# Performance work log

Measured on AMD Instinct MI355X. Metric: run time of the kernel, lower is better.

Reference implementation:

```python
import jax, jax.numpy as jnp
import numpy as np

B, C, H, W = 4, 256, 48, 48
NUM_HEADS = 8
INTER = C // 2          # squeeze_ratio = 2
HEAD_DIM = INTER // NUM_HEADS


def setup_inputs() -> dict:
    key = jax.random.key(0)
    ks = jax.random.split(key, 11)
    s_in = 1.0 / np.sqrt(C)      # torch Conv2d default init scale (uniform bound)
    s_mid = 1.0 / np.sqrt(INTER)
    return {
        "rgb":   jax.random.normal(ks[0], (B, C, H, W), jnp.float32),
        "depth": jax.random.normal(ks[1], (B, C, H, W), jnp.float32),
        "rgbd":  jax.random.normal(ks[2], (B, C, H, W), jnp.float32),
        # 1x1 convs == channel matmuls; store as [out, in] plus bias
        "Wq": jax.random.uniform(ks[3], (INTER, C), jnp.float32, -s_in, s_in),
        "bq": jax.random.uniform(ks[4], (INTER,), jnp.float32, -s_in, s_in),
        "Wk": jax.random.uniform(ks[5], (INTER, C), jnp.float32, -s_in, s_in),
        "bk": jax.random.uniform(ks[6], (INTER,), jnp.float32, -s_in, s_in),
        "Wv": jax.random.uniform(ks[7], (INTER, C), jnp.float32, -s_in, s_in),
        "bv": jax.random.uniform(ks[8], (INTER,), jnp.float32, -s_in, s_in),
        "Wo": jax.random.uniform(ks[9], (C, INTER), jnp.float32, -s_mid, s_mid),
        "bo": jax.random.uniform(ks[10], (C,), jnp.float32, -s_mid, s_mid),
    }


def _proj(x, Wm, bm):
    # 1x1 conv: [B,Cin,H,W] -> [B,Cout,H,W]
    return jnp.einsum('oc,bchw->bohw', Wm, x) + bm[None, :, None, None]


def reference(rgb, depth, rgbd, Wq, bq, Wk, bk, Wv, bv, Wo, bo):
    P = H * W
    # project and split heads: [B, heads, head_dim, P]
    Q = _proj(rgb, Wq, bq).reshape(B, NUM_HEADS, HEAD_DIM, P)
    K = _proj(depth, Wk, bk).reshape(B, NUM_HEADS, HEAD_DIM, P)
    V = _proj(rgbd, Wv, bv).reshape(B, NUM_HEADS, HEAD_DIM, P)
    scale = 1.0 / np.sqrt(HEAD_DIM)
    # scores [B, heads, P(q), P(k)]
    scores = jnp.einsum('bhdq,bhdk->bhqk', Q, K) * scale
    attn = jax.nn.softmax(scores, axis=-1)
    # output [B, heads, head_dim, P(q)] -> [B, INTER, H, W]
    out = jnp.einsum('bhqk,bhdk->bhdq', attn, V).reshape(B, INTER, H, W)
    refined = _proj(out, Wo, bo)
    return (rgb + refined, depth + refined, rgbd + refined)
```

## Files before the change

kernel.cpp:

```cpp
#include <hip/hip_runtime.h>
#include <stdint.h>

#define P_TOT 2304
#define C_IN  256
#define INTER 128
#define NH    8
#define HD    16
#define QSCALE 0.36067376022224087f

typedef short sh4 __attribute__((ext_vector_type(4)));
typedef short sh8 __attribute__((ext_vector_type(8)));
typedef float fl4 __attribute__((ext_vector_type(4)));

static __device__ __forceinline__ unsigned short f2bf(float f) {
    union { float f; unsigned u; } v; v.f = f;
    return (unsigned short)((v.u + 0x7fffu + ((v.u >> 16) & 1u)) >> 16);
}
static __device__ __forceinline__ unsigned pack_bf2(float a, float b) {
    union { float f; unsigned u; } x, y; x.f = a; y.f = b;
    return __builtin_amdgcn_perm(y.u + 0x8000u, x.u + 0x8000u, 0x07060302u);
}
static __device__ __forceinline__ unsigned pack_bf2_trunc(float a, float b) {
    union { float f; unsigned u; } x, y; x.f = a; y.f = b;
    return __builtin_amdgcn_perm(y.u, x.u, 0x07060302u);
}

__global__ __launch_bounds__(256) void k_prep(
    const float* __restrict__ Wq, const float* __restrict__ Wk,
    const float* __restrict__ Wv, const float* __restrict__ Wo,
    unsigned short* __restrict__ Wb) {
    int i = blockIdx.x * 256 + threadIdx.x;
    int seg = i >> 15, off = i & 32767;
    const float* s = (seg == 0 ? Wq : (seg == 1 ? Wk : (seg == 2 ? Wv : Wo)));
    Wb[i] = f2bf(s[off]);
}

__global__ __launch_bounds__(128) void k_qkv(
    const float* __restrict__ rgb, const float* __restrict__ depth,
    const float* __restrict__ rgbd, const unsigned short* __restrict__ Wb,
    const float* __restrict__ bq, const float* __restrict__ bk,
    const float* __restrict__ bv,
    unsigned short* __restrict__ Qt, unsigned short* __restrict__ Kt,
    unsigned short* __restrict__ Vn) {
    int nt = blockIdx.x, pb = blockIdx.y;
    int pr = pb >> 2, b = pb & 3;
    const unsigned short* W = Wb + pr * (INTER * C_IN);
    const float* bias = (pr == 0 ? bq : (pr == 1 ? bk : bv));
    const float* X = (pr == 0 ? rgb : (pr == 1 ? depth : rgbd)) + (size_t)b * C_IN * P_TOT;
    int tid = threadIdx.x, w = tid >> 6, lane = tid & 63;
    int l15 = lane & 15, quad = lane >> 4;
    int p = nt * 32 + w * 16 + l15;
    fl4 zero = {0.f, 0.f, 0.f, 0.f};
    fl4 acc[8];
#pragma unroll
    for (int i = 0; i < 8; ++i) acc[i] = zero;
    const float* xcol = X + p;
    if (pr < 2) {
#pragma unroll
        for (int k0 = 0; k0 < C_IN; k0 += 32) {
            int cb = k0 + quad * 8;
            unsigned u[8];
#pragma unroll
            for (int j = 0; j < 8; ++j) {
                union { float f; unsigned uu; } t;
                t.f = xcol[(size_t)(cb + j) * P_TOT];
                u[j] = t.uu;
            }
            sh8 bfr;
            unsigned* bu = (unsigned*)&bfr;
            bu[0] = __builtin_amdgcn_perm(u[1] + 0x8000u, u[0] + 0x8000u, 0x07060302u);
            bu[1] = __builtin_amdgcn_perm(u[3] + 0x8000u, u[2] + 0x8000u, 0x07060302u);
            bu[2] = __builtin_amdgcn_perm(u[5] + 0x8000u, u[4] + 0x8000u, 0x07060302u);
            bu[3] = __builtin_amdgcn_perm(u[7] + 0x8000u, u[6] + 0x8000u, 0x07060302u);
#pragma unroll
            for (int mf = 0; mf < 8; ++mf) {
                sh8 af = *(const sh8*)(W + (size_t)(mf * 16 + l15) * C_IN + k0 + quad * 8);
                acc[mf] = __builtin_amdgcn_mfma_f32_16x16x32_bf16(af, bfr, acc[mf], 0, 0, 0);
            }
        }
        unsigned short* dst0 = (pr == 0 ? Qt : Kt);
        float sc = (pr == 0 ? QSCALE : 1.0f);
#pragma unroll
        for (int mf = 0; mf < 8; ++mf) {
            float4 bb = *(const float4*)(bias + mf * 16 + quad * 4);
            uint2 v;
            v.x = pack_bf2((acc[mf][0] + bb.x) * sc, (acc[mf][1] + bb.y) * sc);
            v.y = pack_bf2((acc[mf][2] + bb.z) * sc, (acc[mf][3] + bb.w) * sc);
            *(uint2*)(dst0 + ((size_t)(b * NH + mf) * P_TOT + p) * HD + quad * 4) = v;
        }
    } else {
#pragma unroll
        for (int k0 = 0; k0 < C_IN; k0 += 32) {
            int cb = k0 + quad * 8;
            unsigned u[8];
#pragma unroll
            for (int j = 0; j < 8; ++j) {
                union { float f; unsigned uu; } t;
                t.f = xcol[(size_t)(cb + j) * P_TOT];
                u[j] = t.uu;
            }
            sh8 bfr;
            unsigned* bu = (unsigned*)&bfr;
            bu[0] = __builtin_amdgcn_perm(u[1] + 0x8000u, u[0] + 0x8000u, 0x07060302u);
            bu[1] = __builtin_amdgcn_perm(u[3] + 0x8000u, u[2] + 0x8000u, 0x07060302u);
            bu[2] = __builtin_amdgcn_perm(u[5] + 0x8000u, u[4] + 0x8000u, 0x07060302u);
            bu[3] = __builtin_amdgcn_perm(u[7] + 0x8000u, u[6] + 0x8000u, 0x07060302u);
#pragma unroll
            for (int mf = 0; mf < 8; ++mf) {
                sh8 af = *(const sh8*)(W + (size_t)(mf * 16 + l15) * C_IN + k0 + quad * 8);
                acc[mf] = __builtin_amdgcn_mfma_f32_16x16x32_bf16(bfr, af, acc[mf], 0, 0, 0);
            }
        }
        int pv = nt * 32 + w * 16 + quad * 4;
#pragma unroll
        for (int mf = 0; mf < 8; ++mf) {
            float bb = bias[mf * 16 + l15];
            uint2 v;
            v.x = pack_bf2(acc[mf][0] + bb, acc[mf][1] + bb);
            v.y = pack_bf2(acc[mf][2] + bb, acc[mf][3] + bb);
            *(uint2*)(Vn + ((size_t)(b * NH + mf) * HD + l15) * P_TOT + pv) = v;
        }
    }
}

__global__ __launch_bounds__(256) void k_attn(
    const unsigned short* __restrict__ Qt, const unsigned short* __restrict__ Kt,
    const unsigned short* __restrict__ Vn, unsigned short* __restrict__ Ot) {
    __shared__ fl4 ldsO[4][3][64];
    __shared__ fl4 ldsL[3][64];
    int qt = blockIdx.x, h = blockIdx.y, b = blockIdx.z;
    int tid = threadIdx.x, w = tid >> 6, lane = tid & 63;
    int l15 = lane & 15, quad = lane >> 4;
    int bh = b * NH + h;
    int q0 = qt * 64 + l15;
    const unsigned short* qb = Qt + (size_t)bh * P_TOT * HD + quad * 4;
    sh4 qf0 = *(const sh4*)(qb + (size_t)q0 * HD);
    sh4 qf1 = *(const sh4*)(qb + (size_t)(q0 + 16) * HD);
    sh4 qf2 = *(const sh4*)(qb + (size_t)(q0 + 32) * HD);
    sh4 qf3 = *(const sh4*)(qb + (size_t)(q0 + 48) * HD);
    int ko = w * (P_TOT / 4);
    const unsigned short* kb = Kt + (size_t)bh * P_TOT * HD + quad * 4;
    const unsigned short* vb = Vn + ((size_t)bh * HD + l15) * P_TOT + quad * 4;
    fl4 zero = {0.f, 0.f, 0.f, 0.f};
    fl4 o0 = zero, o1 = zero, o2 = zero, o3 = zero;
    fl4 ls = zero;
    for (int kp = ko; kp < ko + P_TOT / 4; kp += 16) {
        sh4 kf = *(const sh4*)(kb + (size_t)(kp + l15) * HD);
        sh4 vf = *(const sh4*)(vb + kp);
        fl4 s0 = __builtin_amdgcn_mfma_f32_16x16x16bf16_1k(kf, qf0, zero, 0, 0, 0);
        fl4 s1 = __builtin_amdgcn_mfma_f32_16x16x16bf16_1k(kf, qf1, zero, 0, 0, 0);
        fl4 s2 = __builtin_amdgcn_mfma_f32_16x16x16bf16_1k(kf, qf2, zero, 0, 0, 0);
        fl4 s3 = __builtin_amdgcn_mfma_f32_16x16x16bf16_1k(kf, qf3, zero, 0, 0, 0);
        float e00 = __builtin_amdgcn_exp2f(s0[0]), e01 = __builtin_amdgcn_exp2f(s0[1]);
        float e02 = __builtin_amdgcn_exp2f(s0[2]), e03 = __builtin_amdgcn_exp2f(s0[3]);
        float e10 = __builtin_amdgcn_exp2f(s1[0]), e11 = __builtin_amdgcn_exp2f(s1[1]);
        float e12 = __builtin_amdgcn_exp2f(s1[2]), e13 = __builtin_amdgcn_exp2f(s1[3]);
        float e20 = __builtin_amdgcn_exp2f(s2[0]), e21 = __builtin_amdgcn_exp2f(s2[1]);
        float e22 = __builtin_amdgcn_exp2f(s2[2]), e23 = __builtin_amdgcn_exp2f(s2[3]);
        float e30 = __builtin_amdgcn_exp2f(s3[0]), e31 = __builtin_amdgcn_exp2f(s3[1]);
        float e32 = __builtin_amdgcn_exp2f(s3[2]), e33 = __builtin_amdgcn_exp2f(s3[3]);
        ls[0] += (e00 + e01) + (e02 + e03);
        ls[1] += (e10 + e11) + (e12 + e13);
        ls[2] += (e20 + e21) + (e22 + e23);
        ls[3] += (e30 + e31) + (e32 + e33);
        sh4 pf0, pf1, pf2, pf3;
        ((unsigned*)&pf0)[0] = pack_bf2_trunc(e00, e01);
        ((unsigned*)&pf0)[1] = pack_bf2_trunc(e02, e03);
        ((unsigned*)&pf1)[0] = pack_bf2_trunc(e10, e11);
        ((unsigned*)&pf1)[1] = pack_bf2_trunc(e12, e13);
        ((unsigned*)&pf2)[0] = pack_bf2_trunc(e20, e21);
        ((unsigned*)&pf2)[1] = pack_bf2_trunc(e22, e23);
        ((unsigned*)&pf3)[0] = pack_bf2_trunc(e30, e31);
        ((unsigned*)&pf3)[1] = pack_bf2_trunc(e32, e33);
        o0 = __builtin_amdgcn_mfma_f32_16x16x16bf16_1k(vf, pf0, o0, 0, 0, 0);
        o1 = __builtin_amdgcn_mfma_f32_16x16x16bf16_1k(vf, pf1, o1, 0, 0, 0);
        o2 = __builtin_amdgcn_mfma_f32_16x16x16bf16_1k(vf, pf2, o2, 0, 0, 0);
        o3 = __builtin_amdgcn_mfma_f32_16x16x16bf16_1k(vf, pf3, o3, 0, 0, 0);
    }
    if (w > 0) {
        ldsO[0][w - 1][lane] = o0;
        ldsO[1][w - 1][lane] = o1;
        ldsO[2][w - 1][lane] = o2;
        ldsO[3][w - 1][lane] = o3;
        ldsL[w - 1][lane] = ls;
    }
    __syncthreads();
    if (w > 0) return;
#pragma unroll
    for (int s = 0; s < 3; ++s) {
        o0 += ldsO[0][s][lane];
        o1 += ldsO[1][s][lane];
        o2 += ldsO[2][s][lane];
        o3 += ldsO[3][s][lane];
        ls += ldsL[s][lane];
    }
#pragma unroll
    for (int i = 0; i < 4; ++i) {
        ls[i] += __shfl_xor(ls[i], 16);
        ls[i] += __shfl_xor(ls[i], 32);
    }
    float i0 = 1.f / ls[0], i1 = 1.f / ls[1], i2 = 1.f / ls[2], i3 = 1.f / ls[3];
    unsigned short* ob = Ot + (size_t)bh * P_TOT * HD + quad * 4;
    uint2 v;
    v.x = pack_bf2(o0[0] * i0, o0[1] * i0); v.y = pack_bf2(o0[2] * i0, o0[3] * i0);
    *(uint2*)(ob + (size_t)q0 * HD) = v;
    v.x = pack_bf2(o1[0] * i1, o1[1] * i1); v.y = pack_bf2(o1[2] * i1, o1[3] * i1);
    *(uint2*)(ob + (size_t)(q0 + 16) * HD) = v;
    v.x = pack_bf2(o2[0] * i2, o2[1] * i2); v.y = pack_bf2(o2[2] * i2, o2[3] * i2);
    *(uint2*)(ob + (size_t)(q0 + 32) * HD) = v;
    v.x = pack_bf2(o3[0] * i3, o3[1] * i3); v.y = pack_bf2(o3[2] * i3, o3[3] * i3);
    *(uint2*)(ob + (size_t)(q0 + 48) * HD) = v;
}

__global__ __launch_bounds__(128) void k_out(
    const unsigned short* __restrict__ Ot, const unsigned short* __restrict__ Wob,
    const float* __restrict__ bo, const float* __restrict__ rgb,
    const float* __restrict__ depth, const float* __restrict__ rgbd,
    float* __restrict__ out) {
    int nt = blockIdx.x, by = blockIdx.y;
    int cz = by >> 2, b = by & 3;
    int tid = threadIdx.x, w = tid >> 6, lane = tid & 63;
    int l15 = lane & 15, quad = lane >> 4;
    int p0 = nt * 16;
    fl4 zero = {0.f, 0.f, 0.f, 0.f};
    fl4 acc[4];
#pragma unroll
    for (int i = 0; i < 4; ++i) acc[i] = zero;
#pragma unroll
    for (int k0 = 0; k0 < INTER; k0 += 32) {
        int h = (k0 >> 4) + (quad >> 1);
        int doff = 8 * (quad & 1);
        sh8 bfr = *(const sh8*)(Ot + ((size_t)(b * NH + h) * P_TOT + p0 + l15) * HD + doff);
#pragma unroll
        for (int mf2 = 0; mf2 < 4; ++mf2) {
            int mf = (cz * 2 + w) * 4 + mf2;
            sh8 af = *(const sh8*)(Wob + (size_t)(mf * 16 + l15) * INTER + k0 + quad * 8);
            acc[mf2] = __builtin_amdgcn_mfma_f32_16x16x32_bf16(bfr, af, acc[mf2], 0, 0, 0);
        }
    }
    const size_t outsz = (size_t)4 * C_IN * P_TOT;
#pragma unroll
    for (int mf2 = 0; mf2 < 4; ++mf2) {
        int ch = ((cz * 2 + w) * 4 + mf2) * 16 + l15;
        float bb = bo[ch];
        size_t idx = ((size_t)b * C_IN + ch) * P_TOT + p0 + quad * 4;
        float r0 = acc[mf2][0] + bb, r1 = acc[mf2][1] + bb;
        float r2 = acc[mf2][2] + bb, r3 = acc[mf2][3] + bb;
        float4 a = *(const float4*)(rgb + idx);
        float4 d = *(const float4*)(depth + idx);
        float4 g = *(const float4*)(rgbd + idx);
        float4 o;
        o.x = a.x + r0; o.y = a.y + r1; o.z = a.z + r2; o.w = a.w + r3;
        *(float4*)(out + idx) = o;
        o.x = d.x + r0; o.y = d.y + r1; o.z = d.z + r2; o.w = d.w + r3;
        *(float4*)(out + outsz + idx) = o;
        o.x = g.x + r0; o.y = g.y + r1; o.z = g.z + r2; o.w = g.w + r3;
        *(float4*)(out + 2 * outsz + idx) = o;
    }
}

extern "C" void kernel_launch(void* const* d_in, const int* in_sizes, int n_in,
                              void* d_out, int out_size, void* d_ws, size_t ws_size,
                              hipStream_t stream) {
    (void)in_sizes; (void)n_in; (void)out_size; (void)ws_size;
    const float* rgb   = (const float*)d_in[0];
    const float* depth = (const float*)d_in[1];
    const float* rgbd  = (const float*)d_in[2];
    const float* Wq = (const float*)d_in[3];
    const float* bq = (const float*)d_in[4];
    const float* Wk = (const float*)d_in[5];
    const float* bk = (const float*)d_in[6];
    const float* Wv = (const float*)d_in[7];
    const float* bv = (const float*)d_in[8];
    const float* Wo = (const float*)d_in[9];
    const float* bo = (const float*)d_in[10];

    float* outp = (float*)d_out;
    unsigned short* Qt = (unsigned short*)d_out;
    unsigned short* Kt = Qt + (size_t)4 * P_TOT * INTER;
    unsigned short* Vn = Kt + (size_t)4 * P_TOT * INTER;
    unsigned short* Ot = (unsigned short*)d_ws;
    unsigned short* Wb = Ot + (size_t)4 * P_TOT * INTER;

    k_prep<<<512, 256, 0, stream>>>(Wq, Wk, Wv, Wo, Wb);
    k_qkv<<<dim3(72, 12), 128, 0, stream>>>(rgb, depth, rgbd, Wb, bq, bk, bv, Qt, Kt, Vn);
    k_attn<<<dim3(36, NH, 4), 256, 0, stream>>>(Qt, Kt, Vn, Ot);
    k_out<<<dim3(144, 8), 128, 0, stream>>>(Ot, Wb + 3 * 32768, bo, rgb, depth, rgbd, outp);
}
```

Baseline: 173.5 us.

## Split QKV reduction across waves, prefetch K/V in attention, widen out-proj parallelism

```diff
diff --git a/kernel.cpp b/kernel.cpp
--- a/kernel.cpp
+++ b/kernel.cpp
@@ -35,49 +35,69 @@
     Wb[i] = f2bf(s[off]);
 }
 
-__global__ __launch_bounds__(128) void k_qkv(
+__global__ __launch_bounds__(256) void k_qkv(
     const float* __restrict__ rgb, const float* __restrict__ depth,
     const float* __restrict__ rgbd, const unsigned short* __restrict__ Wb,
     const float* __restrict__ bq, const float* __restrict__ bk,
     const float* __restrict__ bv,
     unsigned short* __restrict__ Qt, unsigned short* __restrict__ Kt,
     unsigned short* __restrict__ Vn) {
+    __shared__ fl4 ldsA[2][8][64];
     int nt = blockIdx.x, pb = blockIdx.y;
     int pr = pb >> 2, b = pb & 3;
     const unsigned short* W = Wb + pr * (INTER * C_IN);
     const float* bias = (pr == 0 ? bq : (pr == 1 ? bk : bv));
     const float* X = (pr == 0 ? rgb : (pr == 1 ? depth : rgbd)) + (size_t)b * C_IN * P_TOT;
     int tid = threadIdx.x, w = tid >> 6, lane = tid & 63;
+    int wp = w & 1, chalf = w >> 1;
     int l15 = lane & 15, quad = lane >> 4;
-    int p = nt * 32 + w * 16 + l15;
+    int p = nt * 32 + wp * 16 + l15;
     fl4 zero = {0.f, 0.f, 0.f, 0.f};
     fl4 acc[8];
 #pragma unroll
     for (int i = 0; i < 8; ++i) acc[i] = zero;
     const float* xcol = X + p;
-    if (pr < 2) {
-#pragma unroll
-        for (int k0 = 0; k0 < C_IN; k0 += 32) {
-            int cb = k0 + quad * 8;
-            unsigned u[8];
-#pragma unroll
-            for (int j = 0; j < 8; ++j) {
-                union { float f; unsigned uu; } t;
-                t.f = xcol[(size_t)(cb + j) * P_TOT];
-                u[j] = t.uu;
-            }
-            sh8 bfr;
-            unsigned* bu = (unsigned*)&bfr;
-            bu[0] = __builtin_amdgcn_perm(u[1] + 0x8000u, u[0] + 0x8000u, 0x07060302u);
-            bu[1] = __builtin_amdgcn_perm(u[3] + 0x8000u, u[2] + 0x8000u, 0x07060302u);
-            bu[2] = __builtin_amdgcn_perm(u[5] + 0x8000u, u[4] + 0x8000u, 0x07060302u);
-            bu[3] = __builtin_amdgcn_perm(u[7] + 0x8000u, u[6] + 0x8000u, 0x07060302u);
+    int kbeg = chalf * 128;
+#pragma unroll
+    for (int kk = 0; kk < 128; kk += 32) {
+        int k0 = kbeg + kk;
+        int cb = k0 + quad * 8;
+        unsigned u[8];
+#pragma unroll
+        for (int j = 0; j < 8; ++j) {
+            union { float f; unsigned uu; } t;
+            t.f = xcol[(size_t)(cb + j) * P_TOT];
+            u[j] = t.uu;
+        }
+        sh8 bfr;
+        unsigned* bu = (unsigned*)&bfr;
+        bu[0] = __builtin_amdgcn_perm(u[1] + 0x8000u, u[0] + 0x8000u, 0x07060302u);
+        bu[1] = __builtin_amdgcn_perm(u[3] + 0x8000u, u[2] + 0x8000u, 0x07060302u);
+        bu[2] = __builtin_amdgcn_perm(u[5] + 0x8000u, u[4] + 0x8000u, 0x07060302u);
+        bu[3] = __builtin_amdgcn_perm(u[7] + 0x8000u, u[6] + 0x8000u, 0x07060302u);
+        if (pr < 2) {
 #pragma unroll
             for (int mf = 0; mf < 8; ++mf) {
                 sh8 af = *(const sh8*)(W + (size_t)(mf * 16 + l15) * C_IN + k0 + quad * 8);
                 acc[mf] = __builtin_amdgcn_mfma_f32_16x16x32_bf16(af, bfr, acc[mf], 0, 0, 0);
             }
-        }
+        } else {
+#pragma unroll
+            for (int mf = 0; mf < 8; ++mf) {
+                sh8 af = *(const sh8*)(W + (size_t)(mf * 16 + l15) * C_IN + k0 + quad * 8);
+                acc[mf] = __builtin_amdgcn_mfma_f32_16x16x32_bf16(bfr, af, acc[mf], 0, 0, 0);
+            }
+        }
+    }
+    if (chalf == 1) {
+#pragma unroll
+        for (int mf = 0; mf < 8; ++mf) ldsA[wp][mf][lane] = acc[mf];
+    }
+    __syncthreads();
+    if (chalf == 1) return;
+#pragma unroll
+    for (int mf = 0; mf < 8; ++mf) acc[mf] += ldsA[wp][mf][lane];
+    if (pr < 2) {
         unsigned short* dst0 = (pr == 0 ? Qt : Kt);
         float sc = (pr == 0 ? QSCALE : 1.0f);
 #pragma unroll
@@ -89,29 +109,7 @@
             *(uint2*)(dst0 + ((size_t)(b * NH + mf) * P_TOT + p) * HD + quad * 4) = v;
         }
     } else {
-#pragma unroll
-        for (int k0 = 0; k0 < C_IN; k0 += 32) {
-            int cb = k0 + quad * 8;
-            unsigned u[8];
-#pragma unroll
-            for (int j = 0; j < 8; ++j) {
-                union { float f; unsigned uu; } t;
-                t.f = xcol[(size_t)(cb + j) * P_TOT];
-                u[j] = t.uu;
-            }
-            sh8 bfr;
-            unsigned* bu = (unsigned*)&bfr;
-            bu[0] = __builtin_amdgcn_perm(u[1] + 0x8000u, u[0] + 0x8000u, 0x07060302u);
-            bu[1] = __builtin_amdgcn_perm(u[3] + 0x8000u, u[2] + 0x8000u, 0x07060302u);
-            bu[2] = __builtin_amdgcn_perm(u[5] + 0x8000u, u[4] + 0x8000u, 0x07060302u);
-            bu[3] = __builtin_amdgcn_perm(u[7] + 0x8000u, u[6] + 0x8000u, 0x07060302u);
-#pragma unroll
-            for (int mf = 0; mf < 8; ++mf) {
-                sh8 af = *(const sh8*)(W + (size_t)(mf * 16 + l15) * C_IN + k0 + quad * 8);
-                acc[mf] = __builtin_amdgcn_mfma_f32_16x16x32_bf16(bfr, af, acc[mf], 0, 0, 0);
-            }
-        }
-        int pv = nt * 32 + w * 16 + quad * 4;
+        int pv = nt * 32 + wp * 16 + quad * 4;
 #pragma unroll
         for (int mf = 0; mf < 8; ++mf) {
             float bb = bias[mf * 16 + l15];
@@ -139,14 +137,18 @@
     sh4 qf2 = *(const sh4*)(qb + (size_t)(q0 + 32) * HD);
     sh4 qf3 = *(const sh4*)(qb + (size_t)(q0 + 48) * HD);
     int ko = w * (P_TOT / 4);
-    const unsigned short* kb = Kt + (size_t)bh * P_TOT * HD + quad * 4;
-    const unsigned short* vb = Vn + ((size_t)bh * HD + l15) * P_TOT + quad * 4;
+    const unsigned short* kb = Kt + (size_t)bh * P_TOT * HD + (size_t)(ko + l15) * HD + quad * 4;
+    const unsigned short* vb = Vn + ((size_t)bh * HD + l15) * P_TOT + quad * 4 + ko;
     fl4 zero = {0.f, 0.f, 0.f, 0.f};
     fl4 o0 = zero, o1 = zero, o2 = zero, o3 = zero;
     fl4 ls = zero;
-    for (int kp = ko; kp < ko + P_TOT / 4; kp += 16) {
-        sh4 kf = *(const sh4*)(kb + (size_t)(kp + l15) * HD);
-        sh4 vf = *(const sh4*)(vb + kp);
+    const int NIT = P_TOT / 4 / 16;
+    sh4 kf = *(const sh4*)kb;
+    sh4 vf = *(const sh4*)vb;
+    for (int it = 0; it < NIT; ++it) {
+        int nx = (it + 1 < NIT) ? it + 1 : it;
+        sh4 kf_n = *(const sh4*)(kb + (size_t)nx * 16 * HD);
+        sh4 vf_n = *(const sh4*)(vb + nx * 16);
         fl4 s0 = __builtin_amdgcn_mfma_f32_16x16x16bf16_1k(kf, qf0, zero, 0, 0, 0);
         fl4 s1 = __builtin_amdgcn_mfma_f32_16x16x16bf16_1k(kf, qf1, zero, 0, 0, 0);
         fl4 s2 = __builtin_amdgcn_mfma_f32_16x16x16bf16_1k(kf, qf2, zero, 0, 0, 0);
@@ -176,6 +178,8 @@
         o1 = __builtin_amdgcn_mfma_f32_16x16x16bf16_1k(vf, pf1, o1, 0, 0, 0);
         o2 = __builtin_amdgcn_mfma_f32_16x16x16bf16_1k(vf, pf2, o2, 0, 0, 0);
         o3 = __builtin_amdgcn_mfma_f32_16x16x16bf16_1k(vf, pf3, o3, 0, 0, 0);
+        kf = kf_n;
+        vf = vf_n;
     }
     if (w > 0) {
         ldsO[0][w - 1][lane] = o0;
@@ -212,51 +216,41 @@
     *(uint2*)(ob + (size_t)(q0 + 48) * HD) = v;
 }
 
-__global__ __launch_bounds__(128) void k_out(
+__global__ __launch_bounds__(256) void k_out(
     const unsigned short* __restrict__ Ot, const unsigned short* __restrict__ Wob,
     const float* __restrict__ bo, const float* __restrict__ rgb,
     const float* __restrict__ depth, const float* __restrict__ rgbd,
     float* __restrict__ out) {
-    int nt = blockIdx.x, by = blockIdx.y;
-    int cz = by >> 2, b = by & 3;
+    int nt = blockIdx.x, mg = blockIdx.y, b = blockIdx.z;
     int tid = threadIdx.x, w = tid >> 6, lane = tid & 63;
     int l15 = lane & 15, quad = lane >> 4;
+    int mf = mg * 4 + w;
     int p0 = nt * 16;
     fl4 zero = {0.f, 0.f, 0.f, 0.f};
-    fl4 acc[4];
-#pragma unroll
-    for (int i = 0; i < 4; ++i) acc[i] = zero;
+    fl4 acc = zero;
 #pragma unroll
     for (int k0 = 0; k0 < INTER; k0 += 32) {
         int h = (k0 >> 4) + (quad >> 1);
         int doff = 8 * (quad & 1);
         sh8 bfr = *(const sh8*)(Ot + ((size_t)(b * NH + h) * P_TOT + p0 + l15) * HD + doff);
-#pragma unroll
-        for (int mf2 = 0; mf2 < 4; ++mf2) {
-            int mf = (cz * 2 + w) * 4 + mf2;
-            sh8 af = *(const sh8*)(Wob + (size_t)(mf * 16 + l15) * INTER + k0 + quad * 8);
-            acc[mf2] = __builtin_amdgcn_mfma_f32_16x16x32_bf16(bfr, af, acc[mf2], 0, 0, 0);
-        }
+        sh8 af = *(const sh8*)(Wob + (size_t)(mf * 16 + l15) * INTER + k0 + quad * 8);
+        acc = __builtin_amdgcn_mfma_f32_16x16x32_bf16(bfr, af, acc, 0, 0, 0);
     }
     const size_t outsz = (size_t)4 * C_IN * P_TOT;
-#pragma unroll
-    for (int mf2 = 0; mf2 < 4; ++mf2) {
-        int ch = ((cz * 2 + w) * 4 + mf2) * 16 + l15;
-        float bb = bo[ch];
-        size_t idx = ((size_t)b * C_IN + ch) * P_TOT + p0 + quad * 4;
-        float r0 = acc[mf2][0] + bb, r1 = acc[mf2][1] + bb;
-        float r2 = acc[mf2][2] + bb, r3 = acc[mf2][3] + bb;
-        float4 a = *(const float4*)(rgb + idx);
-        float4 d = *(const float4*)(depth + idx);
-        float4 g = *(const float4*)(rgbd + idx);
-        float4 o;
-        o.x = a.x + r0; o.y = a.y + r1; o.z = a.z + r2; o.w = a.w + r3;
-        *(float4*)(out + idx) = o;
-        o.x = d.x + r0; o.y = d.y + r1; o.z = d.z + r2; o.w = d.w + r3;
-        *(float4*)(out + outsz + idx) = o;
-        o.x = g.x + r0; o.y = g.y + r1; o.z = g.z + r2; o.w = g.w + r3;
-        *(float4*)(out + 2 * outsz + idx) = o;
-    }
+    int ch = mf * 16 + l15;
+    float bb = bo[ch];
+    size_t idx = ((size_t)b * C_IN + ch) * P_TOT + p0 + quad * 4;
+    float r0 = acc[0] + bb, r1 = acc[1] + bb, r2 = acc[2] + bb, r3 = acc[3] + bb;
+    float4 a = *(const float4*)(rgb + idx);
+    float4 d = *(const float4*)(depth + idx);
+    float4 g = *(const float4*)(rgbd + idx);
+    float4 o;
+    o.x = a.x + r0; o.y = a.y + r1; o.z = a.z + r2; o.w = a.w + r3;
+    *(float4*)(out + idx) = o;
+    o.x = d.x + r0; o.y = d.y + r1; o.z = d.z + r2; o.w = d.w + r3;
+    *(float4*)(out + outsz + idx) = o;
+    o.x = g.x + r0; o.y = g.y + r1; o.z = g.z + r2; o.w = g.w + r3;
+    *(float4*)(out + 2 * outsz + idx) = o;
 }
 
 extern "C" void kernel_launch(void* const* d_in, const int* in_sizes, int n_in,
@@ -283,7 +277,7 @@
     unsigned short* Wb = Ot + (size_t)4 * P_TOT * INTER;
 
     k_prep<<<512, 256, 0, stream>>>(Wq, Wk, Wv, Wo, Wb);
-    k_qkv<<<dim3(72, 12), 128, 0, stream>>>(rgb, depth, rgbd, Wb, bq, bk, bv, Qt, Kt, Vn);
+    k_qkv<<<dim3(72, 12), 256, 0, stream>>>(rgb, depth, rgbd, Wb, bq, bk, bv, Qt, Kt, Vn);
     k_attn<<<dim3(36, NH, 4), 256, 0, stream>>>(Qt, Kt, Vn, Ot);
-    k_out<<<dim3(144, 8), 128, 0, stream>>>(Ot, Wb + 3 * 32768, bo, rgb, depth, rgbd, outp);
-}
+    k_out<<<dim3(144, 4, 4), 256, 0, stream>>>(Ot, Wb + 3 * 32768, bo, rgb, depth, rgbd, outp);
+}
```

After: 170.0 us. 2.0% less time.
